# Optimization experiments

Measured on AMD Instinct MI355X. Metric: run time of the kernel, lower is better.

Reference implementation:

```python
import jax, jax.numpy as jnp
import numpy as np

EPS = 1e-15
LRELU_ALPHA = 0.2  # = init alpha


def setup_inputs() -> dict:
    key = jax.random.key(0)
    k1, k2, k3, k4 = jax.random.split(key, 4)
    N, E, F_in, F_out = 100000, 3200000, 256, 64
    inputs = jax.random.normal(k1, (N, F_in), dtype=jnp.float32)
    edge_index = jax.random.randint(k2, (2, E), 0, N, dtype=jnp.int64)
    # xavier_normal with gain 1.414
    W = jax.random.normal(k3, (F_in, F_out), dtype=jnp.float32) * (1.414 * np.sqrt(2.0 / (F_in + F_out)))
    a = jax.random.normal(k4, (1, 2 * F_out), dtype=jnp.float32) * (1.414 * np.sqrt(2.0 / (1 + 2 * F_out)))
    return {"inputs": inputs, "edge_index": edge_index, "W": W, "a": a}


def reference(inputs, edge_index, W, a):
    N = inputs.shape[0]
    F_out = W.shape[1]
    src = edge_index[0]  # row i (destination of aggregation)
    dst = edge_index[1]  # col j (neighbor being aggregated)

    h = inputs @ W  # [N, F_out]
    # values = a @ concat(h[src], h[dst]).T  ==  (h @ a1)[src] + (h @ a2)[dst]
    a1 = a[0, :F_out]
    a2 = a[0, F_out:]
    s1 = h @ a1  # [N]
    s2 = h @ a2  # [N]
    values = s1[src] + s2[dst]  # [E]
    ev_a = jax.nn.leaky_relu(values, LRELU_ALPHA)
    edge_value = jnp.exp(ev_a - jnp.max(ev_a))  # global max, as in torch code

    # e_rowsum = A @ ones  -> per-row sum of edge values
    e_rowsum = jax.ops.segment_sum(edge_value, src, num_segments=N)  # [N]
    # h_prime = A @ h (dropout p=0 -> identity)
    h_prime = jax.ops.segment_sum(edge_value[:, None] * h[dst], src, num_segments=N)  # [N, F_out]
    h_prime = h_prime / (e_rowsum[:, None] + EPS)
    return jax.nn.elu(h_prime)  # concat=True
```

## Files before the change

kernel.cpp:

```cpp
#include <hip/hip_runtime.h>
#include <hip/hip_bf16.h>
#include <math.h>

#define F_IN 256
#define F_OUT 64
#define LRELU_ALPHA 0.2f
#define EPS 1e-15f
#define CHUNK 8192
#define BSH 7
#define BNODES 128
#define NBMAX 1024
#define LCAP 4800

typedef __bf16 bf16x8 __attribute__((ext_vector_type(8)));
typedef float  f32x4  __attribute__((ext_vector_type(4)));

__device__ __forceinline__ unsigned int fkey(float x) {
    unsigned int u = __float_as_uint(x);
    return (u & 0x80000000u) ? ~u : (u | 0x80000000u);
}
__device__ __forceinline__ float funkey(unsigned int k) {
    return (k & 0x80000000u) ? __uint_as_float(k ^ 0x80000000u)
                             : __uint_as_float(~k);
}
__device__ __forceinline__ unsigned short f2bf(float x) {
    __hip_bfloat16 b = __float2bfloat16(x);
    return *reinterpret_cast<unsigned short*>(&b);
}
__device__ __forceinline__ float bf2f(unsigned int u) {
    return __uint_as_float(u << 16);
}

__global__ __launch_bounds__(256) void wprep(
    const float* __restrict__ W, unsigned short* __restrict__ Wt)
{
    const int i = blockIdx.x * 256 + threadIdx.x;
    const int n = i & 63;
    const int k = i >> 6;
    Wt[n * 256 + k] = f2bf(W[k * 64 + n]);
}

#define KAP 72
#define KWP 264
__global__ __launch_bounds__(256) void gemm_mfma(
    const float* __restrict__ X, const unsigned short* __restrict__ Wt,
    const float* __restrict__ a,
    unsigned short* __restrict__ h_bf, float* __restrict__ s1,
    float* __restrict__ s2, unsigned int* __restrict__ gsmax, int N)
{
    __shared__ unsigned short As[128 * KAP];
    __shared__ unsigned short Ws[64 * KWP];
    __shared__ float red1[4], red2[4];

    const int tid  = threadIdx.x;
    const int lane = tid & 63;
    const int l15  = lane & 15;
    const int quad = lane >> 4;
    const int w    = tid >> 6;
    const int n0   = blockIdx.x * 128;

#pragma unroll
    for (int i = 0; i < 16; ++i) {
        int q  = tid + i * 256;
        int n  = q >> 6;
        int k4 = q & 63;
        *(uint2*)&Ws[n * KWP + k4 * 4] = *(const uint2*)&Wt[n * 256 + k4 * 4];
    }

    f32x4 acc[2][4] = {};

    for (int c = 0; c < 4; ++c) {
        __syncthreads();
#pragma unroll
        for (int i = 0; i < 8; ++i) {
            int q   = tid + i * 256;
            int row = q >> 4;
            int k4  = q & 15;
            int gr  = n0 + row;
            float4 v = make_float4(0.f, 0.f, 0.f, 0.f);
            if (gr < N)
                v = *(const float4*)&X[(size_t)gr * F_IN + c * 64 + k4 * 4];
            unsigned int p0 = f2bf(v.x) | ((unsigned int)f2bf(v.y) << 16);
            unsigned int p1 = f2bf(v.z) | ((unsigned int)f2bf(v.w) << 16);
            *(uint2*)&As[row * KAP + k4 * 4] = make_uint2(p0, p1);
        }
        __syncthreads();

#pragma unroll
        for (int ks = 0; ks < 64; ks += 32) {
            bf16x8 afrag[2], bfrag[4];
#pragma unroll
            for (int rt = 0; rt < 2; ++rt) {
                uint4 ua = *(const uint4*)&As[(w * 32 + rt * 16 + l15) * KAP + ks + quad * 8];
                afrag[rt] = __builtin_bit_cast(bf16x8, ua);
            }
#pragma unroll
            for (int ct = 0; ct < 4; ++ct) {
                uint4 ub = *(const uint4*)&Ws[(ct * 16 + l15) * KWP + c * 64 + ks + quad * 8];
                bfrag[ct] = __builtin_bit_cast(bf16x8, ub);
            }
#pragma unroll
            for (int rt = 0; rt < 2; ++rt)
#pragma unroll
                for (int ct = 0; ct < 4; ++ct)
                    acc[rt][ct] = __builtin_amdgcn_mfma_f32_16x16x32_bf16(
                        afrag[rt], bfrag[ct], acc[rt][ct], 0, 0, 0);
        }
    }

    float a1v[4], a2v[4];
#pragma unroll
    for (int ct = 0; ct < 4; ++ct) {
        a1v[ct] = a[ct * 16 + l15];
        a2v[ct] = a[F_OUT + ct * 16 + l15];
    }
    float m1 = -INFINITY, m2 = -INFINITY;
#pragma unroll
    for (int rt = 0; rt < 2; ++rt) {
#pragma unroll
        for (int reg = 0; reg < 4; ++reg) {
            int n = n0 + w * 32 + rt * 16 + quad * 4 + reg;
            float p1 = 0.f, p2 = 0.f;
#pragma unroll
            for (int ct = 0; ct < 4; ++ct) {
                float v = acc[rt][ct][reg];
                p1 = fmaf(v, a1v[ct], p1);
                p2 = fmaf(v, a2v[ct], p2);
            }
#pragma unroll
            for (int ofs = 1; ofs < 16; ofs <<= 1) {
                p1 += __shfl_xor(p1, ofs, 64);
                p2 += __shfl_xor(p2, ofs, 64);
            }
            if (n < N) {
#pragma unroll
                for (int ct = 0; ct < 4; ++ct)
                    h_bf[(size_t)n * F_OUT + ct * 16 + l15] = f2bf(acc[rt][ct][reg]);
                if (l15 == 0) { s1[n] = p1; s2[n] = p2; }
                m1 = fmaxf(m1, p1);
                m2 = fmaxf(m2, p2);
            }
        }
    }
#pragma unroll
    for (int ofs = 32; ofs > 0; ofs >>= 1) {
        m1 = fmaxf(m1, __shfl_xor(m1, ofs, 64));
        m2 = fmaxf(m2, __shfl_xor(m2, ofs, 64));
    }
    if (lane == 0) { red1[w] = m1; red2[w] = m2; }
    __syncthreads();
    if (tid == 0) {
        float b1 = fmaxf(fmaxf(red1[0], red1[1]), fmaxf(red1[2], red1[3]));
        float b2 = fmaxf(fmaxf(red2[0], red2[1]), fmaxf(red2[2], red2[3]));
        atomicMax(&gsmax[0], fkey(b1));
        atomicMax(&gsmax[1], fkey(b2));
    }
}

__global__ __launch_bounds__(256) void partition_edges(
    const int* __restrict__ src, const int* __restrict__ dst,
    int* __restrict__ coarse_cnt, unsigned int* __restrict__ coarse,
    int E, int NB)
{
    __shared__ int hist[NBMAX];
    __shared__ int cur[NBMAX];
    const int e0 = blockIdx.x * CHUNK;
    const int e1 = (e0 + CHUNK < E) ? e0 + CHUNK : E;

    for (int i = threadIdx.x; i < NB; i += 256) hist[i] = 0;
    __syncthreads();
    for (int e = e0 + threadIdx.x; e < e1; e += 256)
        atomicAdd(&hist[src[e] >> BSH], 1);
    __syncthreads();
    for (int i = threadIdx.x; i < NB; i += 256) {
        int c = hist[i];
        cur[i] = c ? atomicAdd(&coarse_cnt[i], c) : 0;
    }
    __syncthreads();
    for (int e = e0 + threadIdx.x; e < e1; e += 256) {
        int s = src[e], d = dst[e];
        int b = s >> BSH;
        int pos = atomicAdd(&cur[b], 1);
        if (pos < LCAP)
            coarse[(size_t)b * LCAP + pos] =
                ((unsigned int)d << BSH) | (unsigned int)(s & (BNODES - 1));
    }
}

__global__ __launch_bounds__(512) void bin_gather(
    const unsigned int* __restrict__ coarse, const int* __restrict__ coarse_cnt,
    const float* __restrict__ s1, const float* __restrict__ s2,
    const unsigned int* __restrict__ gsmax,
    const unsigned short* __restrict__ hb, float* __restrict__ out, int N)
{
    __shared__ unsigned int leds[LCAP];
    __shared__ int   hcnt[BNODES];
    __shared__ int   hinc[BNODES];
    __shared__ int   curs[BNODES];
    __shared__ float s1s[BNODES];

    const int b  = blockIdx.x;
    const int t  = threadIdx.x;
    const int n0 = b << BSH;
    int cnt = coarse_cnt[b];
    if (cnt > LCAP) cnt = LCAP;
    const unsigned int* cb = coarse + (size_t)b * LCAP;

    if (t < BNODES) {
        hcnt[t] = 0;
        s1s[t] = (n0 + t < N) ? s1[n0 + t] : 0.f;
    }
    __syncthreads();

    for (int e = t; e < cnt; e += 512)
        atomicAdd(&hcnt[cb[e] & (BNODES - 1)], 1);
    __syncthreads();

    if (t < BNODES) hinc[t] = hcnt[t];
    __syncthreads();
    for (int d = 1; d < BNODES; d <<= 1) {
        int x = (t < BNODES && t >= d) ? hinc[t - d] : 0;
        __syncthreads();
        if (t < BNODES) hinc[t] += x;
        __syncthreads();
    }
    if (t < BNODES) curs[t] = hinc[t] - hcnt[t];
    __syncthreads();

    const float M = funkey(gsmax[0]) + funkey(gsmax[1]);
    for (int e = t; e < cnt; e += 512) {
        unsigned int p = cb[e];
        int sl = p & (BNODES - 1);
        int d  = p >> BSH;
        float v = s1s[sl] + s2[d];
        v = fmaxf(v, LRELU_ALPHA * v);
        float w = __expf(v - M);
        unsigned int wb = f2bf(w);
        int pos = atomicAdd(&curs[sl], 1);
        leds[pos] = ((unsigned int)d << 15) | wb;
    }
    __syncthreads();

    const int lane = t & 63;
    const int wv   = t >> 6;
    const int g    = lane >> 4;
    const int fi   = lane & 15;

    for (int i = 0; i < 16; ++i) {
        const int nl = wv * 16 + i;
        const int n  = n0 + nl;
        const bool valid = (n < N);
        const int re = valid ? hinc[nl] : 0;
        const int rs = valid ? re - hcnt[nl] : 0;

        float a0 = 0.f, a1 = 0.f, a2 = 0.f, a3 = 0.f, ws = 0.f;
        for (int bb = rs; bb < re; bb += 64) {
            const int nb = (re - bb < 64) ? re - bb : 64;
            unsigned int pv = (lane < nb) ? leds[bb + lane] : 0u;
            ws += bf2f(pv & 0x7fffu);
            for (int k = 0; k < nb; k += 4) {
                unsigned int pe = __shfl(pv, k + g, 64);
                float w = bf2f(pe & 0x7fffu);
                uint2 hv = *(const uint2*)&hb[(size_t)(pe >> 15) * F_OUT + fi * 4];
                a0 = fmaf(w, bf2f(hv.x & 0xffffu), a0);
                a1 = fmaf(w, bf2f(hv.x >> 16),     a1);
                a2 = fmaf(w, bf2f(hv.y & 0xffffu), a2);
                a3 = fmaf(w, bf2f(hv.y >> 16),     a3);
            }
        }
        a0 += __shfl_xor(a0, 16, 64); a0 += __shfl_xor(a0, 32, 64);
        a1 += __shfl_xor(a1, 16, 64); a1 += __shfl_xor(a1, 32, 64);
        a2 += __shfl_xor(a2, 16, 64); a2 += __shfl_xor(a2, 32, 64);
        a3 += __shfl_xor(a3, 16, 64); a3 += __shfl_xor(a3, 32, 64);
#pragma unroll
        for (int ofs = 32; ofs > 0; ofs >>= 1)
            ws += __shfl_xor(ws, ofs, 64);

        if (valid && g == 0) {
            float inv = 1.f / (ws + EPS);
            float x0 = a0 * inv, x1 = a1 * inv, x2 = a2 * inv, x3 = a3 * inv;
            x0 = (x0 > 0.f) ? x0 : expm1f(x0);
            x1 = (x1 > 0.f) ? x1 : expm1f(x1);
            x2 = (x2 > 0.f) ? x2 : expm1f(x2);
            x3 = (x3 > 0.f) ? x3 : expm1f(x3);
            *(float4*)&out[(size_t)n * F_OUT + fi * 4] = make_float4(x0, x1, x2, x3);
        }
    }
}

extern "C" void kernel_launch(void* const* d_in, const int* in_sizes, int n_in,
                              void* d_out, int out_size, void* d_ws, size_t ws_size,
                              hipStream_t stream) {
    const float* X   = (const float*)d_in[0];
    const int*   ei  = (const int*)d_in[1];
    const float* W   = (const float*)d_in[2];
    const float* a   = (const float*)d_in[3];
    float*       out = (float*)d_out;

    const int N = in_sizes[0] / F_IN;
    const int E = in_sizes[1] / 2;
    const int* src = ei;
    const int* dst = ei + E;

    const int NB = (N + BNODES - 1) >> BSH;
    const int GB = (N + 127) / 128;
    const int PB = (E + CHUNK - 1) / CHUNK;

    unsigned short* h_bf = (unsigned short*)d_ws;
    float* s1         = (float*)(h_bf + (size_t)N * F_OUT);
    float* s2         = s1 + N;
    int*   coarse_cnt = (int*)(s2 + N);
    unsigned int* gsmax = (unsigned int*)(coarse_cnt + NB);
    unsigned short* Wt = (unsigned short*)(gsmax + 2);
    unsigned int* coarse = (unsigned int*)(Wt + 64 * 256);

    hipMemsetAsync(coarse_cnt, 0, ((size_t)NB + 2) * sizeof(int), stream);

    wprep          <<<64, 256, 0, stream>>>(W, Wt);
    gemm_mfma      <<<GB, 256, 0, stream>>>(X, Wt, a, h_bf, s1, s2, gsmax, N);
    partition_edges<<<PB, 256, 0, stream>>>(src, dst, coarse_cnt, coarse, E, NB);
    bin_gather     <<<NB, 512, 0, stream>>>(coarse, coarse_cnt, s1, s2, gsmax,
                                            h_bf, out, N);
}
```

Baseline: 386.6 us.

## Merge GEMM and edge partition into one launch with block-range dispatch

The independent GEMM and edge-partitioning kernels now share one grid, with the first GB blocks doing the GEMM and the rest partitioning edges, so both run concurrently and one launch is saved. The GEMM no longer stages W in shared memory; it reads B fragments directly from global Wt (cache-resident), which shrinks the LDS footprint to allow more blocks per CU. The cost is that B fragments now come through global/L2 reads, and the two kinds of blocks contend for the same CUs.

Result: faster. 366.2 us (-5.3%).

```diff
diff --git a/kernel.cpp b/kernel.cpp
--- a/kernel.cpp
+++ b/kernel.cpp
@@ -41,149 +41,144 @@
 }
 
 #define KAP 72
-#define KWP 264
-__global__ __launch_bounds__(256) void gemm_mfma(
+__global__ __launch_bounds__(256) void gemm_part(
     const float* __restrict__ X, const unsigned short* __restrict__ Wt,
     const float* __restrict__ a,
     unsigned short* __restrict__ h_bf, float* __restrict__ s1,
-    float* __restrict__ s2, unsigned int* __restrict__ gsmax, int N)
-{
-    __shared__ unsigned short As[128 * KAP];
-    __shared__ unsigned short Ws[64 * KWP];
-    __shared__ float red1[4], red2[4];
-
-    const int tid  = threadIdx.x;
-    const int lane = tid & 63;
-    const int l15  = lane & 15;
-    const int quad = lane >> 4;
-    const int w    = tid >> 6;
-    const int n0   = blockIdx.x * 128;
-
-#pragma unroll
-    for (int i = 0; i < 16; ++i) {
-        int q  = tid + i * 256;
-        int n  = q >> 6;
-        int k4 = q & 63;
-        *(uint2*)&Ws[n * KWP + k4 * 4] = *(const uint2*)&Wt[n * 256 + k4 * 4];
-    }
-
-    f32x4 acc[2][4] = {};
-
-    for (int c = 0; c < 4; ++c) {
-        __syncthreads();
-#pragma unroll
-        for (int i = 0; i < 8; ++i) {
-            int q   = tid + i * 256;
-            int row = q >> 4;
-            int k4  = q & 15;
-            int gr  = n0 + row;
-            float4 v = make_float4(0.f, 0.f, 0.f, 0.f);
-            if (gr < N)
-                v = *(const float4*)&X[(size_t)gr * F_IN + c * 64 + k4 * 4];
-            unsigned int p0 = f2bf(v.x) | ((unsigned int)f2bf(v.y) << 16);
-            unsigned int p1 = f2bf(v.z) | ((unsigned int)f2bf(v.w) << 16);
-            *(uint2*)&As[row * KAP + k4 * 4] = make_uint2(p0, p1);
-        }
-        __syncthreads();
-
-#pragma unroll
-        for (int ks = 0; ks < 64; ks += 32) {
-            bf16x8 afrag[2], bfrag[4];
-#pragma unroll
-            for (int rt = 0; rt < 2; ++rt) {
-                uint4 ua = *(const uint4*)&As[(w * 32 + rt * 16 + l15) * KAP + ks + quad * 8];
-                afrag[rt] = __builtin_bit_cast(bf16x8, ua);
-            }
-#pragma unroll
-            for (int ct = 0; ct < 4; ++ct) {
-                uint4 ub = *(const uint4*)&Ws[(ct * 16 + l15) * KWP + c * 64 + ks + quad * 8];
-                bfrag[ct] = __builtin_bit_cast(bf16x8, ub);
-            }
-#pragma unroll
-            for (int rt = 0; rt < 2; ++rt)
-#pragma unroll
-                for (int ct = 0; ct < 4; ++ct)
-                    acc[rt][ct] = __builtin_amdgcn_mfma_f32_16x16x32_bf16(
-                        afrag[rt], bfrag[ct], acc[rt][ct], 0, 0, 0);
-        }
-    }
-
-    float a1v[4], a2v[4];
-#pragma unroll
-    for (int ct = 0; ct < 4; ++ct) {
-        a1v[ct] = a[ct * 16 + l15];
-        a2v[ct] = a[F_OUT + ct * 16 + l15];
-    }
-    float m1 = -INFINITY, m2 = -INFINITY;
-#pragma unroll
-    for (int rt = 0; rt < 2; ++rt) {
-#pragma unroll
-        for (int reg = 0; reg < 4; ++reg) {
-            int n = n0 + w * 32 + rt * 16 + quad * 4 + reg;
-            float p1 = 0.f, p2 = 0.f;
-#pragma unroll
-            for (int ct = 0; ct < 4; ++ct) {
-                float v = acc[rt][ct][reg];
-                p1 = fmaf(v, a1v[ct], p1);
-                p2 = fmaf(v, a2v[ct], p2);
-            }
-#pragma unroll
-            for (int ofs = 1; ofs < 16; ofs <<= 1) {
-                p1 += __shfl_xor(p1, ofs, 64);
-                p2 += __shfl_xor(p2, ofs, 64);
-            }
-            if (n < N) {
-#pragma unroll
-                for (int ct = 0; ct < 4; ++ct)
-                    h_bf[(size_t)n * F_OUT + ct * 16 + l15] = f2bf(acc[rt][ct][reg]);
-                if (l15 == 0) { s1[n] = p1; s2[n] = p2; }
-                m1 = fmaxf(m1, p1);
-                m2 = fmaxf(m2, p2);
-            }
-        }
-    }
-#pragma unroll
-    for (int ofs = 32; ofs > 0; ofs >>= 1) {
-        m1 = fmaxf(m1, __shfl_xor(m1, ofs, 64));
-        m2 = fmaxf(m2, __shfl_xor(m2, ofs, 64));
-    }
-    if (lane == 0) { red1[w] = m1; red2[w] = m2; }
-    __syncthreads();
-    if (tid == 0) {
-        float b1 = fmaxf(fmaxf(red1[0], red1[1]), fmaxf(red1[2], red1[3]));
-        float b2 = fmaxf(fmaxf(red2[0], red2[1]), fmaxf(red2[2], red2[3]));
-        atomicMax(&gsmax[0], fkey(b1));
-        atomicMax(&gsmax[1], fkey(b2));
-    }
-}
-
-__global__ __launch_bounds__(256) void partition_edges(
+    float* __restrict__ s2, unsigned int* __restrict__ gsmax, int N,
     const int* __restrict__ src, const int* __restrict__ dst,
     int* __restrict__ coarse_cnt, unsigned int* __restrict__ coarse,
-    int E, int NB)
+    int E, int NB, int GB)
 {
-    __shared__ int hist[NBMAX];
-    __shared__ int cur[NBMAX];
-    const int e0 = blockIdx.x * CHUNK;
-    const int e1 = (e0 + CHUNK < E) ? e0 + CHUNK : E;
-
-    for (int i = threadIdx.x; i < NB; i += 256) hist[i] = 0;
-    __syncthreads();
-    for (int e = e0 + threadIdx.x; e < e1; e += 256)
-        atomicAdd(&hist[src[e] >> BSH], 1);
-    __syncthreads();
-    for (int i = threadIdx.x; i < NB; i += 256) {
-        int c = hist[i];
-        cur[i] = c ? atomicAdd(&coarse_cnt[i], c) : 0;
-    }
-    __syncthreads();
-    for (int e = e0 + threadIdx.x; e < e1; e += 256) {
-        int s = src[e], d = dst[e];
-        int b = s >> BSH;
-        int pos = atomicAdd(&cur[b], 1);
-        if (pos < LCAP)
-            coarse[(size_t)b * LCAP + pos] =
-                ((unsigned int)d << BSH) | (unsigned int)(s & (BNODES - 1));
+    __shared__ __align__(16) char smem[18464];
+
+    if (blockIdx.x < GB) {
+        unsigned short* As = (unsigned short*)smem;
+        float* red1 = (float*)(smem + 18432);
+        float* red2 = red1 + 4;
+
+        const int tid  = threadIdx.x;
+        const int lane = tid & 63;
+        const int l15  = lane & 15;
+        const int quad = lane >> 4;
+        const int w    = tid >> 6;
+        const int n0   = blockIdx.x * 128;
+
+        const unsigned short* wbase = Wt + l15 * 256 + quad * 8;
+
+        f32x4 acc[2][4] = {};
+
+        for (int c = 0; c < 4; ++c) {
+            __syncthreads();
+#pragma unroll
+            for (int i = 0; i < 8; ++i) {
+                int q   = tid + i * 256;
+                int row = q >> 4;
+                int k4  = q & 15;
+                int gr  = n0 + row;
+                float4 v = make_float4(0.f, 0.f, 0.f, 0.f);
+                if (gr < N)
+                    v = *(const float4*)&X[(size_t)gr * F_IN + c * 64 + k4 * 4];
+                unsigned int p0 = f2bf(v.x) | ((unsigned int)f2bf(v.y) << 16);
+                unsigned int p1 = f2bf(v.z) | ((unsigned int)f2bf(v.w) << 16);
+                *(uint2*)&As[row * KAP + k4 * 4] = make_uint2(p0, p1);
+            }
+            __syncthreads();
+
+#pragma unroll
+            for (int ks = 0; ks < 64; ks += 32) {
+                bf16x8 afrag[2], bfrag[4];
+#pragma unroll
+                for (int rt = 0; rt < 2; ++rt) {
+                    uint4 ua = *(const uint4*)&As[(w * 32 + rt * 16 + l15) * KAP + ks + quad * 8];
+                    afrag[rt] = __builtin_bit_cast(bf16x8, ua);
+                }
+#pragma unroll
+                for (int ct = 0; ct < 4; ++ct) {
+                    uint4 ub = *(const uint4*)&wbase[ct * 4096 + c * 64 + ks];
+                    bfrag[ct] = __builtin_bit_cast(bf16x8, ub);
+                }
+#pragma unroll
+                for (int rt = 0; rt < 2; ++rt)
+#pragma unroll
+                    for (int ct = 0; ct < 4; ++ct)
+                        acc[rt][ct] = __builtin_amdgcn_mfma_f32_16x16x32_bf16(
+                            afrag[rt], bfrag[ct], acc[rt][ct], 0, 0, 0);
+            }
+        }
+
+        float a1v[4], a2v[4];
+#pragma unroll
+        for (int ct = 0; ct < 4; ++ct) {
+            a1v[ct] = a[ct * 16 + l15];
+            a2v[ct] = a[F_OUT + ct * 16 + l15];
+        }
+        float m1 = -INFINITY, m2 = -INFINITY;
+#pragma unroll
+        for (int rt = 0; rt < 2; ++rt) {
+#pragma unroll
+            for (int reg = 0; reg < 4; ++reg) {
+                int n = n0 + w * 32 + rt * 16 + quad * 4 + reg;
+                float p1 = 0.f, p2 = 0.f;
+#pragma unroll
+                for (int ct = 0; ct < 4; ++ct) {
+                    float v = acc[rt][ct][reg];
+                    p1 = fmaf(v, a1v[ct], p1);
+                    p2 = fmaf(v, a2v[ct], p2);
+                }
+#pragma unroll
+                for (int ofs = 1; ofs < 16; ofs <<= 1) {
+                    p1 += __shfl_xor(p1, ofs, 64);
+                    p2 += __shfl_xor(p2, ofs, 64);
+                }
+                if (n < N) {
+#pragma unroll
+                    for (int ct = 0; ct < 4; ++ct)
+                        h_bf[(size_t)n * F_OUT + ct * 16 + l15] = f2bf(acc[rt][ct][reg]);
+                    if (l15 == 0) { s1[n] = p1; s2[n] = p2; }
+                    m1 = fmaxf(m1, p1);
+                    m2 = fmaxf(m2, p2);
+                }
+            }
+        }
+#pragma unroll
+        for (int ofs = 32; ofs > 0; ofs >>= 1) {
+            m1 = fmaxf(m1, __shfl_xor(m1, ofs, 64));
+            m2 = fmaxf(m2, __shfl_xor(m2, ofs, 64));
+        }
+        if (lane == 0) { red1[w] = m1; red2[w] = m2; }
+        __syncthreads();
+        if (tid == 0) {
+            float b1 = fmaxf(fmaxf(red1[0], red1[1]), fmaxf(red1[2], red1[3]));
+            float b2 = fmaxf(fmaxf(red2[0], red2[1]), fmaxf(red2[2], red2[3]));
+            atomicMax(&gsmax[0], fkey(b1));
+            atomicMax(&gsmax[1], fkey(b2));
+        }
+    } else {
+        int* hist = (int*)smem;
+        int* cur  = hist + NBMAX;
+        const int pb = blockIdx.x - GB;
+        const int e0 = pb * CHUNK;
+        const int e1 = (e0 + CHUNK < E) ? e0 + CHUNK : E;
+
+        for (int i = threadIdx.x; i < NB; i += 256) hist[i] = 0;
+        __syncthreads();
+        for (int e = e0 + threadIdx.x; e < e1; e += 256)
+            atomicAdd(&hist[src[e] >> BSH], 1);
+        __syncthreads();
+        for (int i = threadIdx.x; i < NB; i += 256) {
+            int c = hist[i];
+            cur[i] = c ? atomicAdd(&coarse_cnt[i], c) : 0;
+        }
+        __syncthreads();
+        for (int e = e0 + threadIdx.x; e < e1; e += 256) {
+            int s = src[e], d = dst[e];
+            int b = s >> BSH;
+            int pos = atomicAdd(&cur[b], 1);
+            if (pos < LCAP)
+                coarse[(size_t)b * LCAP + pos] =
+                    ((unsigned int)d << BSH) | (unsigned int)(s & (BNODES - 1));
+        }
     }
 }
 
@@ -316,9 +311,10 @@
 
     hipMemsetAsync(coarse_cnt, 0, ((size_t)NB + 2) * sizeof(int), stream);
 
-    wprep          <<<64, 256, 0, stream>>>(W, Wt);
-    gemm_mfma      <<<GB, 256, 0, stream>>>(X, Wt, a, h_bf, s1, s2, gsmax, N);
-    partition_edges<<<PB, 256, 0, stream>>>(src, dst, coarse_cnt, coarse, E, NB);
-    bin_gather     <<<NB, 512, 0, stream>>>(coarse, coarse_cnt, s1, s2, gsmax,
-                                            h_bf, out, N);
-}
+    wprep     <<<64, 256, 0, stream>>>(W, Wt);
+    gemm_part <<<GB + PB, 256, 0, stream>>>(X, Wt, a, h_bf, s1, s2, gsmax, N,
+                                            src, dst, coarse_cnt, coarse,
+                                            E, NB, GB);
+    bin_gather<<<NB, 512, 0, stream>>>(coarse, coarse_cnt, s1, s2, gsmax,
+                                       h_bf, out, N);
+}
```

## Load GEMM operands directly from global into MFMA fragments, drop LDS staging

Applied to the files above, without the earlier changes.

The projection GEMM no longer stages X and W tiles through shared memory with barriers. Each wave now loads its X rows and the bf16 W fragments straight from global or cache into registers and feeds the MFMAs directly. The block-level max reduction is replaced by per-wave atomics. This removes the LDS traffic and __syncthreads, at the cost of less coalesced X loads and repeated reads of W through the cache.

Measured after the change: 423.0 us. 9.4% more time.

```diff
diff --git a/kernel.cpp b/kernel.cpp
--- a/kernel.cpp
+++ b/kernel.cpp
@@ -40,71 +40,62 @@
     Wt[n * 256 + k] = f2bf(W[k * 64 + n]);
 }
 
-#define KAP 72
-#define KWP 264
-__global__ __launch_bounds__(256) void gemm_mfma(
+__global__ __launch_bounds__(256) void gemm_direct(
     const float* __restrict__ X, const unsigned short* __restrict__ Wt,
     const float* __restrict__ a,
     unsigned short* __restrict__ h_bf, float* __restrict__ s1,
     float* __restrict__ s2, unsigned int* __restrict__ gsmax, int N)
 {
-    __shared__ unsigned short As[128 * KAP];
-    __shared__ unsigned short Ws[64 * KWP];
-    __shared__ float red1[4], red2[4];
-
     const int tid  = threadIdx.x;
     const int lane = tid & 63;
     const int l15  = lane & 15;
     const int quad = lane >> 4;
-    const int w    = tid >> 6;
-    const int n0   = blockIdx.x * 128;
-
-#pragma unroll
-    for (int i = 0; i < 16; ++i) {
-        int q  = tid + i * 256;
-        int n  = q >> 6;
-        int k4 = q & 63;
-        *(uint2*)&Ws[n * KWP + k4 * 4] = *(const uint2*)&Wt[n * 256 + k4 * 4];
-    }
+    const int wv   = tid >> 6;
+    const int n0w  = blockIdx.x * 128 + wv * 32;
+
+    int r0 = n0w + l15;       if (r0 > N - 1) r0 = N - 1;
+    int r1 = n0w + 16 + l15;  if (r1 > N - 1) r1 = N - 1;
+    const float* xrow0 = X + (size_t)r0 * F_IN + quad * 8;
+    const float* xrow1 = X + (size_t)r1 * F_IN + quad * 8;
+    const unsigned short* wb = Wt + l15 * 256 + quad * 8;
 
     f32x4 acc[2][4] = {};
 
+#pragma unroll
     for (int c = 0; c < 4; ++c) {
-        __syncthreads();
-#pragma unroll
-        for (int i = 0; i < 8; ++i) {
-            int q   = tid + i * 256;
-            int row = q >> 4;
-            int k4  = q & 15;
-            int gr  = n0 + row;
-            float4 v = make_float4(0.f, 0.f, 0.f, 0.f);
-            if (gr < N)
-                v = *(const float4*)&X[(size_t)gr * F_IN + c * 64 + k4 * 4];
-            unsigned int p0 = f2bf(v.x) | ((unsigned int)f2bf(v.y) << 16);
-            unsigned int p1 = f2bf(v.z) | ((unsigned int)f2bf(v.w) << 16);
-            *(uint2*)&As[row * KAP + k4 * 4] = make_uint2(p0, p1);
-        }
-        __syncthreads();
-
 #pragma unroll
         for (int ks = 0; ks < 64; ks += 32) {
-            bf16x8 afrag[2], bfrag[4];
-#pragma unroll
-            for (int rt = 0; rt < 2; ++rt) {
-                uint4 ua = *(const uint4*)&As[(w * 32 + rt * 16 + l15) * KAP + ks + quad * 8];
-                afrag[rt] = __builtin_bit_cast(bf16x8, ua);
-            }
+            const int k0 = c * 64 + ks;
+            float4 a0lo = *(const float4*)(xrow0 + k0);
+            float4 a0hi = *(const float4*)(xrow0 + k0 + 4);
+            float4 a1lo = *(const float4*)(xrow1 + k0);
+            float4 a1hi = *(const float4*)(xrow1 + k0 + 4);
+            uint4 ua0 = make_uint4(
+                f2bf(a0lo.x) | ((unsigned int)f2bf(a0lo.y) << 16),
+                f2bf(a0lo.z) | ((unsigned int)f2bf(a0lo.w) << 16),
+                f2bf(a0hi.x) | ((unsigned int)f2bf(a0hi.y) << 16),
+                f2bf(a0hi.z) | ((unsigned int)f2bf(a0hi.w) << 16));
+            uint4 ua1 = make_uint4(
+                f2bf(a1lo.x) | ((unsigned int)f2bf(a1lo.y) << 16),
+                f2bf(a1lo.z) | ((unsigned int)f2bf(a1lo.w) << 16),
+                f2bf(a1hi.x) | ((unsigned int)f2bf(a1hi.y) << 16),
+                f2bf(a1hi.z) | ((unsigned int)f2bf(a1hi.w) << 16));
+            bf16x8 af0 = __builtin_bit_cast(bf16x8, ua0);
+            bf16x8 af1 = __builtin_bit_cast(bf16x8, ua1);
+
+            bf16x8 bfr[4];
 #pragma unroll
             for (int ct = 0; ct < 4; ++ct) {
-                uint4 ub = *(const uint4*)&Ws[(ct * 16 + l15) * KWP + c * 64 + ks + quad * 8];
-                bfrag[ct] = __builtin_bit_cast(bf16x8, ub);
-            }
-#pragma unroll
-            for (int rt = 0; rt < 2; ++rt)
-#pragma unroll
-                for (int ct = 0; ct < 4; ++ct)
-                    acc[rt][ct] = __builtin_amdgcn_mfma_f32_16x16x32_bf16(
-                        afrag[rt], bfrag[ct], acc[rt][ct], 0, 0, 0);
+                uint4 ub = *(const uint4*)&wb[ct * 4096 + k0];
+                bfr[ct] = __builtin_bit_cast(bf16x8, ub);
+            }
+#pragma unroll
+            for (int ct = 0; ct < 4; ++ct) {
+                acc[0][ct] = __builtin_amdgcn_mfma_f32_16x16x32_bf16(
+                    af0, bfr[ct], acc[0][ct], 0, 0, 0);
+                acc[1][ct] = __builtin_amdgcn_mfma_f32_16x16x32_bf16(
+                    af1, bfr[ct], acc[1][ct], 0, 0, 0);
+            }
         }
     }
 
@@ -119,7 +110,7 @@
     for (int rt = 0; rt < 2; ++rt) {
 #pragma unroll
         for (int reg = 0; reg < 4; ++reg) {
-            int n = n0 + w * 32 + rt * 16 + quad * 4 + reg;
+            int n = n0w + rt * 16 + quad * 4 + reg;
             float p1 = 0.f, p2 = 0.f;
 #pragma unroll
             for (int ct = 0; ct < 4; ++ct) {
@@ -147,13 +138,9 @@
         m1 = fmaxf(m1, __shfl_xor(m1, ofs, 64));
         m2 = fmaxf(m2, __shfl_xor(m2, ofs, 64));
     }
-    if (lane == 0) { red1[w] = m1; red2[w] = m2; }
-    __syncthreads();
-    if (tid == 0) {
-        float b1 = fmaxf(fmaxf(red1[0], red1[1]), fmaxf(red1[2], red1[3]));
-        float b2 = fmaxf(fmaxf(red2[0], red2[1]), fmaxf(red2[2], red2[3]));
-        atomicMax(&gsmax[0], fkey(b1));
-        atomicMax(&gsmax[1], fkey(b2));
+    if (lane == 0) {
+        atomicMax(&gsmax[0], fkey(m1));
+        atomicMax(&gsmax[1], fkey(m2));
     }
 }
 
@@ -317,7 +304,7 @@
     hipMemsetAsync(coarse_cnt, 0, ((size_t)NB + 2) * sizeof(int), stream);
 
     wprep          <<<64, 256, 0, stream>>>(W, Wt);
-    gemm_mfma      <<<GB, 256, 0, stream>>>(X, Wt, a, h_bf, s1, s2, gsmax, N);
+    gemm_direct    <<<GB, 256, 0, stream>>>(X, Wt, a, h_bf, s1, s2, gsmax, N);
     partition_edges<<<PB, 256, 0, stream>>>(src, dst, coarse_cnt, coarse, E, NB);
     bin_gather     <<<NB, 512, 0, stream>>>(coarse, coarse_cnt, s1, s2, gsmax,
                                             h_bf, out, N);
```
